# Kernel tuning notes

Measured on AMD Instinct MI355X. Metric: run time of the kernel, lower is better.

Reference implementation:

```python
import jax, jax.numpy as jnp
import numpy as np

B, S, D, H, FF = 2, 2048, 768, 12, 3072
HD = D // H
NEG = -1e9


def _alibi_slopes(n_heads):
    start = 2.0 ** (-8.0 / n_heads)
    return np.array([start ** (i + 1) for i in range(n_heads)], dtype=np.float32)


def setup_inputs() -> dict:
    key = jax.random.key(0)
    ks = jax.random.split(key, 16)
    x = jax.random.normal(ks[0], (B, S, D), dtype=jnp.float32)
    # causal additive mask (seq, seq)
    mask = jnp.where(jnp.tril(jnp.ones((S, S), dtype=bool)), 0.0, NEG).astype(jnp.float32)
    # ALiBi bias (n_heads, seq, seq): slope * -(i - j) for j <= i
    slopes = jnp.asarray(_alibi_slopes(H))  # (H,)
    rel = jnp.arange(S)[None, :] - jnp.arange(S)[:, None]  # (S,S), j - i
    alibi_bias = (slopes[:, None, None] * rel[None, :, :]).astype(jnp.float32)
    sc = 0.02
    p = {
        'wq': jax.random.normal(ks[1], (D, D)) * sc, 'bq': jnp.zeros((D,)),
        'wk': jax.random.normal(ks[2], (D, D)) * sc, 'bk': jnp.zeros((D,)),
        'wv': jax.random.normal(ks[3], (D, D)) * sc, 'bv': jnp.zeros((D,)),
        'wo': jax.random.normal(ks[4], (D, D)) * sc, 'bo': jnp.zeros((D,)),
        'w1': jax.random.normal(ks[5], (FF, D)) * sc, 'b1': jnp.zeros((FF,)),
        'w2': jax.random.normal(ks[6], (D, FF)) * sc, 'b2': jnp.zeros((D,)),
        'g1': jnp.ones((D,)), 'be1': jnp.zeros((D,)),
        'g2': jnp.ones((D,)), 'be2': jnp.zeros((D,)),
    }
    return {'x': x, 'mask': mask, 'alibi_bias': alibi_bias, **p}


def _ln(x, g, b, eps=1e-5):
    mu = jnp.mean(x, axis=-1, keepdims=True)
    var = jnp.mean((x - mu) ** 2, axis=-1, keepdims=True)
    return (x - mu) * jax.lax.rsqrt(var + eps) * g + b


def reference(x, mask, alibi_bias, wq, bq, wk, bk, wv, bv, wo, bo,
              w1, b1, w2, b2, g1, be1, g2, be2):
    b, s, _ = x.shape
    def split_heads(t):
        return t.reshape(b, s, H, HD).transpose(0, 2, 1, 3)  # (B,H,S,HD)
    q = split_heads(x @ wq.T + bq)
    k = split_heads(x @ wk.T + bk)
    v = split_heads(x @ wv.T + bv)
    scores = jnp.einsum('bhqd,bhkd->bhqk', q, k) / jnp.sqrt(jnp.float32(HD))
    scores = scores + alibi_bias[None] + mask[None, None]
    attn = jax.nn.softmax(scores, axis=-1)
    out = jnp.einsum('bhqk,bhkd->bhqd', attn, v)
    out = out.transpose(0, 2, 1, 3).reshape(b, s, D)
    out = out @ wo.T + bo
    x = _ln(x + out, g1, be1)
    ff = jax.nn.relu(x @ w1.T + b1) @ w2.T + b2
    x = _ln(x + ff, g2, be2)
    return x
```

## Files before the change

kernel.cpp:

```cpp
#include <hip/hip_runtime.h>
#include <math.h>

#define BB   2
#define SS   2048
#define DD   768
#define HH   12
#define HDIM 64
#define FFD  3072

typedef __attribute__((ext_vector_type(8))) short bf16x8;
typedef __attribute__((ext_vector_type(4))) float f32x4;

__device__ __forceinline__ unsigned short f2bf(float f) {
  unsigned u = __float_as_uint(f);
  u += 0x7fffu + ((u >> 16) & 1u);
  return (unsigned short)(u >> 16);
}
__device__ __forceinline__ float bf2f(unsigned short s) {
  return __uint_as_float(((unsigned)s) << 16);
}

__device__ __forceinline__ void glb2lds16(const void* g, void* l) {
  __builtin_amdgcn_global_load_lds(
      (const __attribute__((address_space(1))) unsigned int*)g,
      (__attribute__((address_space(3))) unsigned int*)l, 16, 0, 0);
}

__global__ __launch_bounds__(256) void cast_bf16_kernel(
    const float* __restrict__ in, unsigned short* __restrict__ out, int n) {
  int i = (blockIdx.x * 256 + threadIdx.x) * 4;
  if (i < n) {
    float4 f = *(const float4*)&in[i];
    ushort4 o;
    o.x = f2bf(f.x); o.y = f2bf(f.y); o.z = f2bf(f.z); o.w = f2bf(f.w);
    *(ushort4*)&out[i] = o;
  }
}

enum { EP_QKV3_BF16 = 0, EP_RELU_BF16 = 1, EP_F32_PART = 2, EP_BF16_PART = 3 };

template <int EPI, int SPLITK>
__global__ __launch_bounds__(256) void gemm_bt(
    const unsigned short* __restrict__ A, const unsigned short* __restrict__ W,
    const float* __restrict__ bias, const float* __restrict__ biasK,
    const float* __restrict__ biasV, void* __restrict__ C0,
    void* __restrict__ C1, void* __restrict__ C2,
    int M, int N, int K) {
  __shared__ unsigned short Alds[128 * 32];
  __shared__ unsigned short Blds[128 * 32];
  const int bm = blockIdx.y * 128, bn = blockIdx.x * 128;
  const int t = threadIdx.x;
  const int lane = t & 63, wid = t >> 6;
  const int wm = (wid >> 1) * 64, wn = (wid & 1) * 64;
  const int r16 = lane & 15, q4 = lane >> 4;
  const int klen = K / SPLITK;
  const int kbeg = (SPLITK > 1) ? blockIdx.z * klen : 0;
  const int kend = kbeg + klen;

  f32x4 acc[4][4] = {};

  for (int k0 = kbeg; k0 < kend; k0 += 32) {
    __syncthreads();
    #pragma unroll
    for (int l = 0; l < 2; ++l) {
      int c = t + l * 256;
      int row = c >> 2;
      int kq = (c & 3) ^ ((row >> 1) & 3);
      int base = ((t & 192) + l * 256) * 8;
      glb2lds16(&A[(size_t)(bm + row) * K + k0 + 8 * kq], &Alds[base]);
      glb2lds16(&W[(size_t)(bn + row) * K + k0 + 8 * kq], &Blds[base]);
    }
    __syncthreads();
    bf16x8 af[4], bfv[4];
    #pragma unroll
    for (int i = 0; i < 4; ++i) {
      int row = wm + i * 16 + r16;
      af[i] = *(const bf16x8*)&Alds[(row * 4 + (q4 ^ ((row >> 1) & 3))) * 8];
    }
    #pragma unroll
    for (int j = 0; j < 4; ++j) {
      int row = wn + j * 16 + r16;
      bfv[j] = *(const bf16x8*)&Blds[(row * 4 + (q4 ^ ((row >> 1) & 3))) * 8];
    }
    #pragma unroll
    for (int i = 0; i < 4; ++i)
      #pragma unroll
      for (int j = 0; j < 4; ++j)
        acc[i][j] = __builtin_amdgcn_mfma_f32_16x16x32_bf16(af[i], bfv[j], acc[i][j], 0, 0, 0);
  }

  #pragma unroll
  for (int i = 0; i < 4; ++i) {
    #pragma unroll
    for (int j = 0; j < 4; ++j) {
      #pragma unroll
      for (int r = 0; r < 4; ++r) {
        int m = bm + wm + i * 16 + q4 * 4 + r;
        int n = bn + wn + j * 16 + r16;
        float val = acc[i][j][r];
        if (EPI == EP_QKV3_BF16) {
          int mat = (n >= 1536) ? 2 : (n >= 768 ? 1 : 0);
          int c = n - mat * 768;
          const float* bp = (mat == 0) ? bias : (mat == 1 ? biasK : biasV);
          val += bp[c];
          int b = m >> 11, s = m & 2047;
          int h = c >> 6, hd = c & 63;
          unsigned short* dst = (unsigned short*)(mat == 0 ? C0 : (mat == 1 ? C1 : C2));
          dst[(((size_t)b * HH + h) * SS + s) * HDIM + hd] = f2bf(val);
        } else if (EPI == EP_RELU_BF16) {
          val += bias[n];
          ((unsigned short*)C0)[(size_t)m * N + n] = f2bf(fmaxf(val, 0.f));
        } else if (EPI == EP_F32_PART) {
          ((float*)C0)[(size_t)blockIdx.z * M * N + (size_t)m * N + n] = val;
        } else {
          ((unsigned short*)C0)[(size_t)blockIdx.z * M * N + (size_t)m * N + n] = f2bf(val);
        }
      }
    }
  }
}

#define VSTR 72

__global__ __launch_bounds__(256) void attn5_kernel(
    const unsigned short* __restrict__ Q, const unsigned short* __restrict__ K,
    const unsigned short* __restrict__ V, unsigned short* __restrict__ Opart,
    float* __restrict__ Lpart) {
  __shared__ unsigned short Kl[2][64 * 64];
  __shared__ unsigned short Vt[64 * VSTR];
  __shared__ unsigned short Pl[4][16 * VSTR];

  const int qt = (SS / 64 - 1) - blockIdx.x;
  const int bh = blockIdx.y;
  const int z  = blockIdx.z;
  const int h = bh % HH;
  const int b = bh / HH;
  const int t = threadIdx.x;
  const int lane = t & 63, w = t >> 6;
  const int r16 = lane & 15, q4 = lane >> 4;
  const float k1 = 0.125f * 1.44269504f;
  const float slope2 = exp2f(-8.0f * (float)(h + 1) / 12.0f) * 1.44269504f;
  const int qg0 = qt * 64 + w * 16;

  const int nt = qt + 1;
  const int bsz = nt >> 2, rem = nt & 3;
  const int cnt = bsz + (z < rem ? 1 : 0);
  const int lo = z * bsz + (z < rem ? z : rem);
  const int hi = lo + cnt;

  bf16x8 qf[2];
  {
    const unsigned short* qbase = Q + ((size_t)bh * SS + qg0) * HDIM;
    #pragma unroll
    for (int ks = 0; ks < 2; ++ks)
      qf[ks] = *(const bf16x8*)(qbase + r16 * HDIM + ks * 32 + q4 * 8);
  }

  f32x4 O[4] = {};
  float rs[4] = {};

  const unsigned short* Kb = K + (size_t)bh * SS * HDIM;
  const unsigned short* Vb = V + (size_t)bh * SS * HDIM;
  const int kp = t & 31, dq = t >> 5;
  bf16x8 v0r, v1r;

  if (cnt > 0) {
    const unsigned short* kg = Kb + (size_t)lo * 64 * HDIM;
    #pragma unroll
    for (int l = 0; l < 2; ++l) {
      int c = t + l * 256;
      int key = c >> 3, kq = (c & 7) ^ (key & 7);
      glb2lds16(&kg[key * HDIM + 8 * kq], &Kl[lo & 1][((t & 192) + l * 256) * 8]);
    }
    const unsigned short* vg = Vb + (size_t)lo * 64 * HDIM;
    v0r = *(const bf16x8*)(vg + (2 * kp) * HDIM + dq * 8);
    v1r = *(const bf16x8*)(vg + (2 * kp + 1) * HDIM + dq * 8);
  }

  for (int kt = lo; kt < hi; ++kt) {
    __syncthreads();
    #pragma unroll
    for (int e = 0; e < 8; ++e) {
      unsigned u = ((unsigned)(unsigned short)v0r[e]) |
                   (((unsigned)(unsigned short)v1r[e]) << 16);
      *(unsigned*)&Vt[(dq * 8 + e) * VSTR + 2 * kp] = u;
    }
    __syncthreads();
    if (kt + 1 < hi) {
      const unsigned short* kg = Kb + (size_t)(kt + 1) * 64 * HDIM;
      #pragma unroll
      for (int l = 0; l < 2; ++l) {
        int c = t + l * 256;
        int key = c >> 3, kq = (c & 7) ^ (key & 7);
        glb2lds16(&kg[key * HDIM + 8 * kq],
                  &Kl[(kt + 1) & 1][((t & 192) + l * 256) * 8]);
      }
      const unsigned short* vg = Vb + (size_t)(kt + 1) * 64 * HDIM;
      v0r = *(const bf16x8*)(vg + (2 * kp) * HDIM + dq * 8);
      v1r = *(const bf16x8*)(vg + (2 * kp + 1) * HDIM + dq * 8);
    }
    const unsigned short* Kt = Kl[kt & 1];

    f32x4 sc[4] = {};
    #pragma unroll
    for (int ks = 0; ks < 2; ++ks) {
      bf16x8 kf[4];
      #pragma unroll
      for (int jb = 0; jb < 4; ++jb) {
        int key = jb * 16 + r16;
        kf[jb] = *(const bf16x8*)&Kt[(key * 8 + ((ks * 4 + q4) ^ (key & 7))) * 8];
      }
      #pragma unroll
      for (int jb = 0; jb < 4; ++jb)
        sc[jb] = __builtin_amdgcn_mfma_f32_16x16x32_bf16(qf[ks], kf[jb], sc[jb], 0, 0, 0);
    }

    #pragma unroll
    for (int r = 0; r < 4; ++r) {
      int qrow = qg0 + q4 * 4 + r;
      int d0 = kt * 64 + r16 - qrow;
      #pragma unroll
      for (int jb = 0; jb < 4; ++jb) {
        int diff = d0 + jb * 16;
        float p = (diff <= 0) ? exp2f(sc[jb][r] * k1 + slope2 * (float)diff) : 0.f;
        rs[r] += p;
        Pl[w][(q4 * 4 + r) * VSTR + jb * 16 + r16] = f2bf(p);
      }
    }

    #pragma unroll
    for (int ks = 0; ks < 2; ++ks) {
      bf16x8 pf = *(const bf16x8*)&Pl[w][r16 * VSTR + ks * 32 + q4 * 8];
      bf16x8 vf[4];
      #pragma unroll
      for (int jb = 0; jb < 4; ++jb)
        vf[jb] = *(const bf16x8*)&Vt[(jb * 16 + r16) * VSTR + ks * 32 + q4 * 8];
      #pragma unroll
      for (int jb = 0; jb < 4; ++jb)
        O[jb] = __builtin_amdgcn_mfma_f32_16x16x32_bf16(pf, vf[jb], O[jb], 0, 0, 0);
    }
  }

  #pragma unroll
  for (int r = 0; r < 4; ++r) {
    float lsum = rs[r];
    #pragma unroll
    for (int off = 1; off < 16; off <<= 1) lsum += __shfl_xor(lsum, off, 64);
    int qg = qg0 + q4 * 4 + r;
    if (r16 == 0)
      Lpart[((size_t)z * BB * HH + bh) * SS + qg] = lsum;
    unsigned short* ob = Opart + (size_t)z * BB * SS * DD +
                         ((size_t)b * SS + qg) * DD + h * HDIM;
    #pragma unroll
    for (int jb = 0; jb < 4; ++jb)
      ob[jb * 16 + r16] = f2bf(O[jb][r]);
  }
}

__global__ __launch_bounds__(256) void attn_combine_kernel(
    const unsigned short* __restrict__ Opart, const float* __restrict__ Lpart,
    unsigned short* __restrict__ at) {
  const size_t i = ((size_t)blockIdx.x * 256 + threadIdx.x) * 4;
  const int d = (int)(i % DD);
  const int sg = (int)(i / DD);
  const int b = sg >> 11, s = sg & 2047;
  const int h = d >> 6;
  const size_t zstr = (size_t)BB * SS * DD;
  float l = 0.f;
  #pragma unroll
  for (int zz = 0; zz < 4; ++zz)
    l += Lpart[((size_t)zz * BB * HH + b * HH + h) * SS + s];
  float inv = 1.f / l;
  float acc4[4] = {};
  #pragma unroll
  for (int zz = 0; zz < 4; ++zz) {
    ushort4 o4 = *(const ushort4*)&Opart[zz * zstr + i];
    acc4[0] += bf2f(o4.x); acc4[1] += bf2f(o4.y);
    acc4[2] += bf2f(o4.z); acc4[3] += bf2f(o4.w);
  }
  ushort4 r;
  r.x = f2bf(acc4[0] * inv); r.y = f2bf(acc4[1] * inv);
  r.z = f2bf(acc4[2] * inv); r.w = f2bf(acc4[3] * inv);
  *(ushort4*)&at[i] = r;
}

__global__ __launch_bounds__(256) void ln1_kernel(
    const float* __restrict__ x, const float* __restrict__ p,
    const float* __restrict__ bo, const float* __restrict__ g,
    const float* __restrict__ be, unsigned short* __restrict__ outb) {
  const int row = blockIdx.x, t = threadIdx.x;
  const size_t base = (size_t)row * DD;
  const size_t str = (size_t)BB * SS * DD;
  float v[3];
  float s = 0.f;
  #pragma unroll
  for (int i = 0; i < 3; ++i) {
    int c = t + i * 256;
    v[i] = x[base + c] + p[base + c] + p[str + base + c] + bo[c];
    s += v[i];
  }
  __shared__ float red[256];
  red[t] = s; __syncthreads();
  for (int off = 128; off > 0; off >>= 1) { if (t < off) red[t] += red[t + off]; __syncthreads(); }
  float mu = red[0] * (1.0f / DD);
  __syncthreads();
  float s2 = 0.f;
  #pragma unroll
  for (int i = 0; i < 3; ++i) { float d = v[i] - mu; s2 += d * d; }
  red[t] = s2; __syncthreads();
  for (int off = 128; off > 0; off >>= 1) { if (t < off) red[t] += red[t + off]; __syncthreads(); }
  float rstd = rsqrtf(red[0] * (1.0f / DD) + 1e-5f);
  #pragma unroll
  for (int i = 0; i < 3; ++i) {
    int c = t + i * 256;
    outb[base + c] = f2bf((v[i] - mu) * rstd * g[c] + be[c]);
  }
}

__global__ __launch_bounds__(256) void ln2_kernel(
    const unsigned short* __restrict__ a, const unsigned short* __restrict__ f,
    const float* __restrict__ b2, const float* __restrict__ g,
    const float* __restrict__ be, float* __restrict__ out) {
  const int row = blockIdx.x, t = threadIdx.x;
  const size_t base = (size_t)row * DD;
  const size_t str = (size_t)BB * SS * DD;
  float v[3];
  float s = 0.f;
  #pragma unroll
  for (int i = 0; i < 3; ++i) {
    int c = t + i * 256;
    size_t ix = base + c;
    v[i] = bf2f(a[ix]) + bf2f(f[ix]) + bf2f(f[str + ix]) +
           bf2f(f[2 * str + ix]) + bf2f(f[3 * str + ix]) + b2[c];
    s += v[i];
  }
  __shared__ float red[256];
  red[t] = s; __syncthreads();
  for (int off = 128; off > 0; off >>= 1) { if (t < off) red[t] += red[t + off]; __syncthreads(); }
  float mu = red[0] * (1.0f / DD);
  __syncthreads();
  float s2 = 0.f;
  #pragma unroll
  for (int i = 0; i < 3; ++i) { float d = v[i] - mu; s2 += d * d; }
  red[t] = s2; __syncthreads();
  for (int off = 128; off > 0; off >>= 1) { if (t < off) red[t] += red[t + off]; __syncthreads(); }
  float rstd = rsqrtf(red[0] * (1.0f / DD) + 1e-5f);
  #pragma unroll
  for (int i = 0; i < 3; ++i) {
    int c = t + i * 256;
    out[base + c] = (v[i] - mu) * rstd * g[c] + be[c];
  }
}

extern "C" void kernel_launch(void* const* d_in, const int* in_sizes, int n_in,
                              void* d_out, int out_size, void* d_ws, size_t ws_size,
                              hipStream_t stream) {
  const float* x   = (const float*)d_in[0];
  const float* wq  = (const float*)d_in[3];
  const float* bq  = (const float*)d_in[4];
  const float* wk  = (const float*)d_in[5];
  const float* bk  = (const float*)d_in[6];
  const float* wv  = (const float*)d_in[7];
  const float* bv  = (const float*)d_in[8];
  const float* wo  = (const float*)d_in[9];
  const float* bo  = (const float*)d_in[10];
  const float* w1  = (const float*)d_in[11];
  const float* b1  = (const float*)d_in[12];
  const float* w2  = (const float*)d_in[13];
  const float* b2  = (const float*)d_in[14];
  const float* g1  = (const float*)d_in[15];
  const float* be1 = (const float*)d_in[16];
  const float* g2  = (const float*)d_in[17];
  const float* be2 = (const float*)d_in[18];
  float* out = (float*)d_out;

  char* ws = (char*)d_ws;
  unsigned short* wqkvb = (unsigned short*)(ws + 0);
  unsigned short* wob   = (unsigned short*)(ws + 3538944);
  unsigned short* w1b   = (unsigned short*)(ws + 4718592);
  unsigned short* w2b   = (unsigned short*)(ws + 9437184);
  unsigned short* xb    = (unsigned short*)(ws + 14155776);
  unsigned short* qb    = (unsigned short*)(ws + 20456448);
  unsigned short* kb    = (unsigned short*)(ws + 26747904);
  unsigned short* vb    = (unsigned short*)(ws + 33039360);
  unsigned short* at    = (unsigned short*)(ws + 39330816);
  unsigned short* opart = (unsigned short*)(ws + 45622272);
  float*          lpart = (float*)(ws + 14155776);
  float*          pj    = (float*)(ws + 14155776);
  unsigned short* x1b   = (unsigned short*)(ws + 39330816);
  unsigned short* f1    = (unsigned short*)(ws + 45622272);
  unsigned short* f2b   = (unsigned short*)(ws + 14155776);

  const int M = BB * SS;
  dim3 blk(256);

  cast_bf16_kernel<<<dim3(M * DD / 1024), blk, 0, stream>>>(x, xb, M * DD);
  cast_bf16_kernel<<<dim3(DD * DD / 1024), blk, 0, stream>>>(wq, wqkvb, DD * DD);
  cast_bf16_kernel<<<dim3(DD * DD / 1024), blk, 0, stream>>>(wk, wqkvb + DD * DD, DD * DD);
  cast_bf16_kernel<<<dim3(DD * DD / 1024), blk, 0, stream>>>(wv, wqkvb + 2 * DD * DD, DD * DD);
  cast_bf16_kernel<<<dim3(DD * DD / 1024), blk, 0, stream>>>(wo, wob, DD * DD);
  cast_bf16_kernel<<<dim3(FFD * DD / 1024), blk, 0, stream>>>(w1, w1b, FFD * DD);
  cast_bf16_kernel<<<dim3(FFD * DD / 1024), blk, 0, stream>>>(w2, w2b, FFD * DD);

  gemm_bt<EP_QKV3_BF16, 1><<<dim3(3 * DD / 128, M / 128, 1), blk, 0, stream>>>(
      xb, wqkvb, bq, bk, bv, qb, kb, vb, M, 3 * DD, DD);

  attn5_kernel<<<dim3(SS / 64, BB * HH, 4), blk, 0, stream>>>(qb, kb, vb, opart, lpart);
  attn_combine_kernel<<<dim3(M * DD / 1024), blk, 0, stream>>>(opart, lpart, at);

  gemm_bt<EP_F32_PART, 2><<<dim3(DD / 128, M / 128, 2), blk, 0, stream>>>(
      at, wob, nullptr, nullptr, nullptr, pj, nullptr, nullptr, M, DD, DD);

  ln1_kernel<<<dim3(M), blk, 0, stream>>>(x, pj, bo, g1, be1, x1b);

  gemm_bt<EP_RELU_BF16, 1><<<dim3(FFD / 128, M / 128, 1), blk, 0, stream>>>(
      x1b, w1b, b1, nullptr, nullptr, f1, nullptr, nullptr, M, FFD, DD);

  gemm_bt<EP_BF16_PART, 4><<<dim3(DD / 128, M / 128, 4), blk, 0, stream>>>(
      f1, w2b, nullptr, nullptr, nullptr, f2b, nullptr, nullptr, M, DD, FFD);

  ln2_kernel<<<dim3(M), blk, 0, stream>>>(x1b, f2b, b2, g2, be2, out);
}
```

Baseline: 506.1 us.

## Double-buffer GEMM and attention LDS, fuse casts, use shuffle-based LayerNorm reductions

The seven fp32-to-bf16 cast launches become one segmented cast kernel. The GEMM gets double-buffered LDS tiles so the next K-slice loads while MFMAs run. Attention double-buffers the V-transpose tile, which removes one barrier per key tile. Both LayerNorm kernels switch to a single-pass sum and sum-of-squares with a wave-shuffle reduction, which cuts barriers but computes variance as E[x²]−mu², a form that is less numerically robust.

```diff
diff --git a/kernel.cpp b/kernel.cpp
--- a/kernel.cpp
+++ b/kernel.cpp
@@ -26,15 +26,22 @@
       (__attribute__((address_space(3))) unsigned int*)l, 16, 0, 0);
 }
 
-__global__ __launch_bounds__(256) void cast_bf16_kernel(
-    const float* __restrict__ in, unsigned short* __restrict__ out, int n) {
-  int i = (blockIdx.x * 256 + threadIdx.x) * 4;
-  if (i < n) {
-    float4 f = *(const float4*)&in[i];
-    ushort4 o;
-    o.x = f2bf(f.x); o.y = f2bf(f.y); o.z = f2bf(f.z); o.w = f2bf(f.w);
-    *(ushort4*)&out[i] = o;
-  }
+struct CastSegs {
+  const float* src[7];
+  unsigned short* dst[7];
+  int cum[8];
+};
+
+__global__ __launch_bounds__(256) void cast_all_kernel(CastSegs segs, int total4) {
+  int i = blockIdx.x * 256 + threadIdx.x;
+  if (i >= total4) return;
+  int s = 0;
+  while (i >= segs.cum[s + 1]) ++s;
+  int off = (i - segs.cum[s]) * 4;
+  float4 f = *(const float4*)&segs.src[s][off];
+  ushort4 o;
+  o.x = f2bf(f.x); o.y = f2bf(f.y); o.z = f2bf(f.z); o.w = f2bf(f.w);
+  *(ushort4*)&segs.dst[s][off] = o;
 }
 
 enum { EP_QKV3_BF16 = 0, EP_RELU_BF16 = 1, EP_F32_PART = 2, EP_BF16_PART = 3 };
@@ -46,11 +53,12 @@
     const float* __restrict__ biasV, void* __restrict__ C0,
     void* __restrict__ C1, void* __restrict__ C2,
     int M, int N, int K) {
-  __shared__ unsigned short Alds[128 * 32];
-  __shared__ unsigned short Blds[128 * 32];
+  __shared__ unsigned short Alds[2][128 * 32];
+  __shared__ unsigned short Blds[2][128 * 32];
   const int bm = blockIdx.y * 128, bn = blockIdx.x * 128;
   const int t = threadIdx.x;
-  const int lane = t & 63, wid = t >> 6;
+  const int lane = t & 63;
+  const int wid = t >> 6;
   const int wm = (wid >> 1) * 64, wn = (wid & 1) * 64;
   const int r16 = lane & 15, q4 = lane >> 4;
   const int klen = K / SPLITK;
@@ -59,34 +67,40 @@
 
   f32x4 acc[4][4] = {};
 
-  for (int k0 = kbeg; k0 < kend; k0 += 32) {
-    __syncthreads();
+  auto stage = [&](int k0, int b) {
     #pragma unroll
     for (int l = 0; l < 2; ++l) {
       int c = t + l * 256;
       int row = c >> 2;
       int kq = (c & 3) ^ ((row >> 1) & 3);
       int base = ((t & 192) + l * 256) * 8;
-      glb2lds16(&A[(size_t)(bm + row) * K + k0 + 8 * kq], &Alds[base]);
-      glb2lds16(&W[(size_t)(bn + row) * K + k0 + 8 * kq], &Blds[base]);
-    }
+      glb2lds16(&A[(size_t)(bm + row) * K + k0 + 8 * kq], &Alds[b][base]);
+      glb2lds16(&W[(size_t)(bn + row) * K + k0 + 8 * kq], &Blds[b][base]);
+    }
+  };
+
+  stage(kbeg, 0);
+  int buf = 0;
+  for (int k0 = kbeg; k0 < kend; k0 += 32) {
     __syncthreads();
+    if (k0 + 32 < kend) stage(k0 + 32, buf ^ 1);
     bf16x8 af[4], bfv[4];
     #pragma unroll
     for (int i = 0; i < 4; ++i) {
       int row = wm + i * 16 + r16;
-      af[i] = *(const bf16x8*)&Alds[(row * 4 + (q4 ^ ((row >> 1) & 3))) * 8];
+      af[i] = *(const bf16x8*)&Alds[buf][(row * 4 + (q4 ^ ((row >> 1) & 3))) * 8];
     }
     #pragma unroll
     for (int j = 0; j < 4; ++j) {
       int row = wn + j * 16 + r16;
-      bfv[j] = *(const bf16x8*)&Blds[(row * 4 + (q4 ^ ((row >> 1) & 3))) * 8];
+      bfv[j] = *(const bf16x8*)&Blds[buf][(row * 4 + (q4 ^ ((row >> 1) & 3))) * 8];
     }
     #pragma unroll
     for (int i = 0; i < 4; ++i)
       #pragma unroll
       for (int j = 0; j < 4; ++j)
         acc[i][j] = __builtin_amdgcn_mfma_f32_16x16x32_bf16(af[i], bfv[j], acc[i][j], 0, 0, 0);
+    buf ^= 1;
   }
 
   #pragma unroll
@@ -127,7 +141,7 @@
     const unsigned short* __restrict__ V, unsigned short* __restrict__ Opart,
     float* __restrict__ Lpart) {
   __shared__ unsigned short Kl[2][64 * 64];
-  __shared__ unsigned short Vt[64 * VSTR];
+  __shared__ unsigned short Vt[2][64 * VSTR];
   __shared__ unsigned short Pl[4][16 * VSTR];
 
   const int qt = (SS / 64 - 1) - blockIdx.x;
@@ -164,37 +178,34 @@
   const int kp = t & 31, dq = t >> 5;
   bf16x8 v0r, v1r;
 
-  if (cnt > 0) {
-    const unsigned short* kg = Kb + (size_t)lo * 64 * HDIM;
+  auto stageK = [&](int kt) {
+    const unsigned short* kg = Kb + (size_t)kt * 64 * HDIM;
     #pragma unroll
     for (int l = 0; l < 2; ++l) {
       int c = t + l * 256;
       int key = c >> 3, kq = (c & 7) ^ (key & 7);
-      glb2lds16(&kg[key * HDIM + 8 * kq], &Kl[lo & 1][((t & 192) + l * 256) * 8]);
-    }
+      glb2lds16(&kg[key * HDIM + 8 * kq], &Kl[kt & 1][((t & 192) + l * 256) * 8]);
+    }
+  };
+
+  if (cnt > 0) {
+    stageK(lo);
     const unsigned short* vg = Vb + (size_t)lo * 64 * HDIM;
     v0r = *(const bf16x8*)(vg + (2 * kp) * HDIM + dq * 8);
     v1r = *(const bf16x8*)(vg + (2 * kp + 1) * HDIM + dq * 8);
   }
 
   for (int kt = lo; kt < hi; ++kt) {
-    __syncthreads();
+    unsigned short* Vtc = Vt[kt & 1];
     #pragma unroll
     for (int e = 0; e < 8; ++e) {
       unsigned u = ((unsigned)(unsigned short)v0r[e]) |
                    (((unsigned)(unsigned short)v1r[e]) << 16);
-      *(unsigned*)&Vt[(dq * 8 + e) * VSTR + 2 * kp] = u;
+      *(unsigned*)&Vtc[(dq * 8 + e) * VSTR + 2 * kp] = u;
     }
     __syncthreads();
     if (kt + 1 < hi) {
-      const unsigned short* kg = Kb + (size_t)(kt + 1) * 64 * HDIM;
-      #pragma unroll
-      for (int l = 0; l < 2; ++l) {
-        int c = t + l * 256;
-        int key = c >> 3, kq = (c & 7) ^ (key & 7);
-        glb2lds16(&kg[key * HDIM + 8 * kq],
-                  &Kl[(kt + 1) & 1][((t & 192) + l * 256) * 8]);
-      }
+      stageK(kt + 1);
       const unsigned short* vg = Vb + (size_t)(kt + 1) * 64 * HDIM;
       v0r = *(const bf16x8*)(vg + (2 * kp) * HDIM + dq * 8);
       v1r = *(const bf16x8*)(vg + (2 * kp + 1) * HDIM + dq * 8);
@@ -234,7 +245,7 @@
       bf16x8 vf[4];
       #pragma unroll
       for (int jb = 0; jb < 4; ++jb)
-        vf[jb] = *(const bf16x8*)&Vt[(jb * 16 + r16) * VSTR + ks * 32 + q4 * 8];
+        vf[jb] = *(const bf16x8*)&Vtc[(jb * 16 + r16) * VSTR + ks * 32 + q4 * 8];
       #pragma unroll
       for (int jb = 0; jb < 4; ++jb)
         O[jb] = __builtin_amdgcn_mfma_f32_16x16x32_bf16(pf, vf[jb], O[jb], 0, 0, 0);
@@ -284,6 +295,19 @@
   *(ushort4*)&at[i] = r;
 }
 
+__device__ __forceinline__ void block_reduce2(float& s1, float& s2, int t) {
+  __shared__ float red[8];
+  #pragma unroll
+  for (int off = 1; off < 64; off <<= 1) {
+    s1 += __shfl_xor(s1, off, 64);
+    s2 += __shfl_xor(s2, off, 64);
+  }
+  if ((t & 63) == 0) { red[(t >> 6) * 2] = s1; red[(t >> 6) * 2 + 1] = s2; }
+  __syncthreads();
+  s1 = red[0] + red[2] + red[4] + red[6];
+  s2 = red[1] + red[3] + red[5] + red[7];
+}
+
 __global__ __launch_bounds__(256) void ln1_kernel(
     const float* __restrict__ x, const float* __restrict__ p,
     const float* __restrict__ bo, const float* __restrict__ g,
@@ -292,24 +316,16 @@
   const size_t base = (size_t)row * DD;
   const size_t str = (size_t)BB * SS * DD;
   float v[3];
-  float s = 0.f;
+  float s1 = 0.f, s2 = 0.f;
   #pragma unroll
   for (int i = 0; i < 3; ++i) {
     int c = t + i * 256;
     v[i] = x[base + c] + p[base + c] + p[str + base + c] + bo[c];
-    s += v[i];
-  }
-  __shared__ float red[256];
-  red[t] = s; __syncthreads();
-  for (int off = 128; off > 0; off >>= 1) { if (t < off) red[t] += red[t + off]; __syncthreads(); }
-  float mu = red[0] * (1.0f / DD);
-  __syncthreads();
-  float s2 = 0.f;
-  #pragma unroll
-  for (int i = 0; i < 3; ++i) { float d = v[i] - mu; s2 += d * d; }
-  red[t] = s2; __syncthreads();
-  for (int off = 128; off > 0; off >>= 1) { if (t < off) red[t] += red[t + off]; __syncthreads(); }
-  float rstd = rsqrtf(red[0] * (1.0f / DD) + 1e-5f);
+    s1 += v[i]; s2 += v[i] * v[i];
+  }
+  block_reduce2(s1, s2, t);
+  float mu = s1 * (1.0f / DD);
+  float rstd = rsqrtf(s2 * (1.0f / DD) - mu * mu + 1e-5f);
   #pragma unroll
   for (int i = 0; i < 3; ++i) {
     int c = t + i * 256;
@@ -325,26 +341,18 @@
   const size_t base = (size_t)row * DD;
   const size_t str = (size_t)BB * SS * DD;
   float v[3];
-  float s = 0.f;
+  float s1 = 0.f, s2 = 0.f;
   #pragma unroll
   for (int i = 0; i < 3; ++i) {
     int c = t + i * 256;
     size_t ix = base + c;
     v[i] = bf2f(a[ix]) + bf2f(f[ix]) + bf2f(f[str + ix]) +
            bf2f(f[2 * str + ix]) + bf2f(f[3 * str + ix]) + b2[c];
-    s += v[i];
-  }
-  __shared__ float red[256];
-  red[t] = s; __syncthreads();
-  for (int off = 128; off > 0; off >>= 1) { if (t < off) red[t] += red[t + off]; __syncthreads(); }
-  float mu = red[0] * (1.0f / DD);
-  __syncthreads();
-  float s2 = 0.f;
-  #pragma unroll
-  for (int i = 0; i < 3; ++i) { float d = v[i] - mu; s2 += d * d; }
-  red[t] = s2; __syncthreads();
-  for (int off = 128; off > 0; off >>= 1) { if (t < off) red[t] += red[t + off]; __syncthreads(); }
-  float rstd = rsqrtf(red[0] * (1.0f / DD) + 1e-5f);
+    s1 += v[i]; s2 += v[i] * v[i];
+  }
+  block_reduce2(s1, s2, t);
+  float mu = s1 * (1.0f / DD);
+  float rstd = rsqrtf(s2 * (1.0f / DD) - mu * mu + 1e-5f);
   #pragma unroll
   for (int i = 0; i < 3; ++i) {
     int c = t + i * 256;
@@ -394,13 +402,21 @@
   const int M = BB * SS;
   dim3 blk(256);
 
-  cast_bf16_kernel<<<dim3(M * DD / 1024), blk, 0, stream>>>(x, xb, M * DD);
-  cast_bf16_kernel<<<dim3(DD * DD / 1024), blk, 0, stream>>>(wq, wqkvb, DD * DD);
-  cast_bf16_kernel<<<dim3(DD * DD / 1024), blk, 0, stream>>>(wk, wqkvb + DD * DD, DD * DD);
-  cast_bf16_kernel<<<dim3(DD * DD / 1024), blk, 0, stream>>>(wv, wqkvb + 2 * DD * DD, DD * DD);
-  cast_bf16_kernel<<<dim3(DD * DD / 1024), blk, 0, stream>>>(wo, wob, DD * DD);
-  cast_bf16_kernel<<<dim3(FFD * DD / 1024), blk, 0, stream>>>(w1, w1b, FFD * DD);
-  cast_bf16_kernel<<<dim3(FFD * DD / 1024), blk, 0, stream>>>(w2, w2b, FFD * DD);
+  CastSegs cs;
+  cs.src[0] = x;  cs.dst[0] = xb;
+  cs.src[1] = wq; cs.dst[1] = wqkvb;
+  cs.src[2] = wk; cs.dst[2] = wqkvb + DD * DD;
+  cs.src[3] = wv; cs.dst[3] = wqkvb + 2 * DD * DD;
+  cs.src[4] = wo; cs.dst[4] = wob;
+  cs.src[5] = w1; cs.dst[5] = w1b;
+  cs.src[6] = w2; cs.dst[6] = w2b;
+  {
+    int n[7] = {M * DD, DD * DD, DD * DD, DD * DD, DD * DD, FFD * DD, FFD * DD};
+    int c = 0;
+    for (int i = 0; i < 7; ++i) { cs.cum[i] = c; c += n[i] / 4; }
+    cs.cum[7] = c;
+    cast_all_kernel<<<dim3((c + 255) / 256), blk, 0, stream>>>(cs, c);
+  }
 
   gemm_bt<EP_QKV3_BF16, 1><<<dim3(3 * DD / 128, M / 128, 1), blk, 0, stream>>>(
       xb, wqkvb, bq, bk, bv, qb, kb, vb, M, 3 * DD, DD);
```

After: 492.2 us. -2.7%, faster.
